# Kernel optimization log

Measured on AMD Instinct MI355X. Metric: run time of the kernel, lower is better.

## Reference

```python
import jax, jax.numpy as jnp
import numpy as np

C = 256
N_HEAD = 4
GROUPS = 32
EPS = 1e-5
B, H, W = 2, 64, 64


def group_norm(x, gamma, beta):
    # x: [B, C, H, W]; GroupNorm over (C//G, H, W) within each group
    b, c, h, w = x.shape
    xr = x.reshape(b, GROUPS, c // GROUPS, h, w)
    m = xr.mean(axis=(2, 3, 4), keepdims=True)
    v = xr.var(axis=(2, 3, 4), keepdims=True)
    xn = ((xr - m) * jax.lax.rsqrt(v + EPS)).reshape(b, c, h, w)
    return xn * gamma[None, :, None, None] + beta[None, :, None, None]


def setup_inputs() -> dict:
    key = jax.random.key(0)
    ks = jax.random.split(key, 5)
    s = 1.0 / np.sqrt(C)  # fan-in init scale for 1x1 convs
    return {
        "input": jax.random.normal(ks[0], (B, C, H, W), jnp.float32),
        "c": jax.random.normal(ks[1], (B, C, H, W), jnp.float32),
        "gn_w": jnp.ones((C,), jnp.float32),
        "gn_b": jnp.zeros((C,), jnp.float32),
        "wq": jax.random.normal(ks[2], (C, C), jnp.float32) * s,
        "wkv": jax.random.normal(ks[3], (2 * C, C), jnp.float32) * s,
        "wout_w": jax.random.normal(ks[4], (C, C), jnp.float32) * s,
        "wout_b": jnp.zeros((C,), jnp.float32),
    }


def reference(input, c, gn_w, gn_b, wq, wkv, wout_w, wout_b):
    b, ch, h, w = input.shape
    hd = ch // N_HEAD
    n = h * w
    # shared GroupNorm applied to both query source and context
    nq = group_norm(input, gn_w, gn_b)
    nkv = group_norm(c, gn_w, gn_b)
    # 1x1 convs == channel matmuls
    q = jnp.einsum('oc,bchw->bohw', wq, nq).reshape(b, N_HEAD, hd, n)
    kv = jnp.einsum('oc,bchw->bohw', wkv, nkv).reshape(b, N_HEAD, 2 * hd, n)
    k, v = jnp.split(kv, 2, axis=2)  # each [b, nh, hd, n]
    # NOTE: scale is 1/sqrt(channel), as in the source (not 1/sqrt(head_dim))
    attn = jnp.einsum('bncq,bnck->bnqk', q, k) / jnp.sqrt(jnp.float32(ch))
    attn = jax.nn.softmax(attn, axis=-1)
    o = jnp.einsum('bnqk,bnck->bncq', attn, v).reshape(b, ch, h, w)
    o = jnp.einsum('oc,bchw->bohw', wout_w, o) + wout_b[None, :, None, None]
    return o + input
```

## Files before the change

### kernel.cpp

```cpp
#include <hip/hip_runtime.h>


typedef __attribute__((ext_vector_type(8))) short short8;
typedef __attribute__((ext_vector_type(4))) short s4;
typedef __attribute__((ext_vector_type(4))) float f32x4;
typedef __attribute__((ext_vector_type(2))) unsigned int uint2v;

__device__ __forceinline__ unsigned short f2bf(float x) {
    unsigned int u = __builtin_bit_cast(unsigned int, x);
    u += 0x7FFFu + ((u >> 16) & 1u);
    return (unsigned short)(u >> 16);
}

__device__ __forceinline__ unsigned int pk2(float a, float b) {
    unsigned int ua = __builtin_bit_cast(unsigned int, a) + 0x8000u;
    unsigned int ub = __builtin_bit_cast(unsigned int, b) + 0x8000u;
    return (ua >> 16) | (ub & 0xFFFF0000u);
}

__device__ __forceinline__ short8 ld8(const unsigned short* p) {
    return *reinterpret_cast<const short8*>(p);
}

#define MFMA(a, b, c) __builtin_amdgcn_mfma_f32_16x16x32_bf16((a), (b), (c), 0, 0, 0)
#define MFMA16(a, b, c) __builtin_amdgcn_mfma_f32_16x16x16bf16_1k((a), (b), (c), 0, 0, 0)

__global__ __launch_bounds__(256) void wcvt(const float* __restrict__ wq,
                                            const float* __restrict__ wkv,
                                            const float* __restrict__ wo,
                                            unsigned short* __restrict__ dst) {
    int i = blockIdx.x * 256 + threadIdx.x;
    float v;
    if (i < 65536)       v = wq[i];
    else if (i < 196608) v = wkv[i - 65536];
    else                 v = wo[i - 196608];
    dst[i] = f2bf(v);
}

__global__ __launch_bounds__(256) void gnorm(const float* __restrict__ x0,
                                             const float* __restrict__ x1,
                                             unsigned short* __restrict__ d0,
                                             unsigned short* __restrict__ d1,
                                             const float* __restrict__ gamma,
                                             const float* __restrict__ beta) {
    int bid = blockIdx.x;
    const float* x = (bid & 64) ? x1 : x0;
    unsigned short* dst = (bid & 64) ? d1 : d0;
    int b = (bid >> 5) & 1, g = bid & 31;
    const float* base = x + (size_t)(b * 256 + g * 8) * 4096;
    int tid = threadIdx.x, lane = tid & 63, w = tid >> 6;

    float s = 0.f, s2 = 0.f;
    const float4* b4 = (const float4*)base;
    for (int i = tid; i < 8192; i += 256) {
        float4 v = b4[i];
        s  += v.x + v.y + v.z + v.w;
        s2 += v.x * v.x + v.y * v.y + v.z * v.z + v.w * v.w;
    }
    #pragma unroll
    for (int off = 32; off; off >>= 1) {
        s  += __shfl_down(s, off);
        s2 += __shfl_down(s2, off);
    }
    __shared__ float red[8];
    __shared__ float stat[2];
    if (lane == 0) { red[w] = s; red[4 + w] = s2; }
    __syncthreads();
    if (tid == 0) {
        float S = red[0] + red[1] + red[2] + red[3];
        float S2 = red[4] + red[5] + red[6] + red[7];
        float mean = S * (1.f / 32768.f);
        float var = S2 * (1.f / 32768.f) - mean * mean;
        stat[0] = mean;
        stat[1] = rsqrtf(var + 1e-5f);
    }
    __syncthreads();
    float mean = stat[0], inv = stat[1];

    float a[8], c0[8];
    #pragma unroll
    for (int cl = 0; cl < 8; cl++) {
        float gm = gamma[g * 8 + cl], bt = beta[g * 8 + cl];
        a[cl]  = gm * inv;
        c0[cl] = bt - mean * gm * inv;
    }
    for (int n = tid; n < 4096; n += 256) {
        unsigned short o[8];
        #pragma unroll
        for (int cl = 0; cl < 8; cl++) {
            float v = base[cl * 4096 + n];
            o[cl] = f2bf(v * a[cl] + c0[cl]);
        }
        *(uint4*)&dst[((size_t)(b * 4096 + n)) * 256 + g * 8] = *(const uint4*)o;
    }
}

__global__ __launch_bounds__(256) void proj_all(const unsigned short* __restrict__ nqT,
                                                const unsigned short* __restrict__ nkvT,
                                                const unsigned short* __restrict__ Wq,
                                                const unsigned short* __restrict__ Wkv,
                                                unsigned short* __restrict__ QT,
                                                unsigned short* __restrict__ KF,
                                                unsigned short* __restrict__ VF) {
    int bb = blockIdx.z;
    int y = blockIdx.y;
    bool isQ = (y < 4);
    int n0 = blockIdx.x * 128;
    int o0 = (isQ ? y : (y - 4)) * 64;
    int w = threadIdx.x >> 6, lane = threadIdx.x & 63;
    int m16 = lane & 15, g = lane >> 4;
    const unsigned short* Xb = (isQ ? nqT : nkvT) + (size_t)bb * 4096 * 256;
    const unsigned short* W = isQ ? Wq : Wkv;
    f32x4 acc[2][4] = {};
    int rowA = n0 + w * 32 + m16;
    #pragma unroll
    for (int k0 = 0; k0 < 256; k0 += 32) {
        short8 a0 = ld8(Xb + (size_t)rowA * 256 + k0 + g * 8);
        short8 a1 = ld8(Xb + (size_t)(rowA + 16) * 256 + k0 + g * 8);
        #pragma unroll
        for (int ct = 0; ct < 4; ct++) {
            short8 bf = ld8(W + (size_t)(o0 + ct * 16 + m16) * 256 + k0 + g * 8);
            acc[0][ct] = MFMA(a0, bf, acc[0][ct]);
            acc[1][ct] = MFMA(a1, bf, acc[1][ct]);
        }
    }
    if (isQ) {
        unsigned short* Ob = QT + (size_t)bb * 4096 * 256;
        #pragma unroll
        for (int mt = 0; mt < 2; mt++)
            #pragma unroll
            for (int ct = 0; ct < 4; ct++)
                #pragma unroll
                for (int r = 0; r < 4; r++) {
                    int n = n0 + w * 32 + mt * 16 + g * 4 + r;
                    int o = o0 + ct * 16 + m16;
                    Ob[(size_t)n * 256 + o] = f2bf(acc[mt][ct][r] * 0.0625f);
                }
    } else {
        int h2 = o0 >> 7, isV = (o0 >> 6) & 1;
        int bh = bb * 4 + h2;
        unsigned short* base = (isV ? VF : KF) + (size_t)bh * 262144;
        #pragma unroll
        for (int mt = 0; mt < 2; mt++)
            #pragma unroll
            for (int ct = 0; ct < 4; ct++)
                #pragma unroll
                for (int r = 0; r < 4; r++) {
                    int n = n0 + w * 32 + mt * 16 + g * 4 + r;
                    int c = ct * 16 + m16;
                    unsigned short v = f2bf(acc[mt][ct][r]);
                    size_t off;
                    if (isV) {
                        int T32 = n >> 5, kk5 = n & 31;
                        int gg = (kk5 & 15) >> 2;
                        int j = (kk5 & 3) + ((kk5 >> 4) << 2);
                        off = (((size_t)(T32 * 4 + ct)) * 64 + ((c & 15) + 16 * gg)) * 8 + j;
                    } else {
                        int T16 = n >> 4;
                        int cb = c >> 5, gg = (c >> 3) & 3, e = c & 7;
                        off = (((size_t)(T16 * 2 + cb)) * 64 + ((n & 15) + 16 * gg)) * 8 + e;
                    }
                    base[off] = v;
                }
    }
}

__global__ __launch_bounds__(512, 2) void attn(const unsigned short* __restrict__ QT,
                                               const unsigned short* __restrict__ KF,
                                               const unsigned short* __restrict__ VF,
                                               unsigned short* __restrict__ OT) {
    __shared__ unsigned short sm[32768];
    int bh = blockIdx.x & 7;
    int qb = blockIdx.x >> 3;
    int bb = bh >> 2, h = bh & 3;
    int tid = threadIdx.x;
    int w = tid >> 6, lane = tid & 63;
    int wq = w & 3, hh = w >> 2;
    int m16 = lane & 15, g = lane >> 4;
    int tloc = tid & 255;

    const unsigned short* KFb = KF + (size_t)bh * 262144;
    const unsigned short* VFb = VF + (size_t)bh * 262144;
    const unsigned short* Qb = QT + (size_t)bb * 4096 * 256;

    int q0 = qb * 64 + wq * 16;
    short8 bq0 = ld8(Qb + (size_t)(q0 + m16) * 256 + h * 64 + g * 8);
    short8 bq1 = ld8(Qb + (size_t)(q0 + m16) * 256 + h * 64 + 32 + g * 8);

    f32x4 acc[4] = {};
    float l = 0.f;

    {
        const uint4* ks = (const uint4*)(KFb + (size_t)(hh * 128) * 1024) + tloc;
        const uint4* vs = (const uint4*)(VFb + (size_t)(hh * 64) * 2048) + tloc;
        uint4 k0 = ks[0], k1 = ks[256], v0 = vs[0], v1 = vs[256];
        uint4* kd = (uint4*)(sm + (hh * 2) * 4096) + tloc;
        uint4* vd = (uint4*)(sm + 16384 + (hh * 2) * 4096) + tloc;
        kd[0] = k0; kd[256] = k1; vd[0] = v0; vd[256] = v1;
    }
    __syncthreads();

    for (int it = 0; it < 32; ++it) {
        int p = it & 1;
        bool pf = (it + 1 < 32);
        uint4 kp0, kp1, vp0, vp1;
        if (pf) {
            const uint4* ks = (const uint4*)(KFb + (size_t)(hh * 128 + (it + 1) * 4) * 1024) + tloc;
            const uint4* vs = (const uint4*)(VFb + (size_t)(hh * 64 + (it + 1) * 2) * 2048) + tloc;
            kp0 = ks[0]; kp1 = ks[256]; vp0 = vs[0]; vp1 = vs[256];
        }

        const unsigned short* Kbuf = sm + (hh * 2 + p) * 4096;
        const unsigned short* Vbuf = sm + 16384 + (hh * 2 + p) * 4096;

        s4 pb[4];
        #pragma unroll
        for (int t16 = 0; t16 < 4; t16++) {
            short8 a0 = ld8(Kbuf + (t16 * 2 + 0) * 512 + lane * 8);
            short8 a1 = ld8(Kbuf + (t16 * 2 + 1) * 512 + lane * 8);
            f32x4 st = {};
            st = MFMA(a0, bq0, st);
            st = MFMA(a1, bq1, st);
            #pragma unroll
            for (int r = 0; r < 4; r++) st[r] = __expf(st[r]);
            l += (st[0] + st[1]) + (st[2] + st[3]);
            uint2v wv; wv.x = pk2(st[0], st[1]); wv.y = pk2(st[2], st[3]);
            pb[t16] = __builtin_bit_cast(s4, wv);
        }
        #pragma unroll
        for (int T32 = 0; T32 < 2; T32++)
            #pragma unroll
            for (int dt = 0; dt < 4; dt++) {
                short8 va = ld8(Vbuf + (T32 * 4 + dt) * 512 + lane * 8);
                s4 va0 = __builtin_shufflevector(va, va, 0, 1, 2, 3);
                s4 va1 = __builtin_shufflevector(va, va, 4, 5, 6, 7);
                acc[dt] = MFMA16(va0, pb[T32 * 2], acc[dt]);
                acc[dt] = MFMA16(va1, pb[T32 * 2 + 1], acc[dt]);
            }

        if (pf) {
            uint4* kd = (uint4*)(sm + (hh * 2 + (p ^ 1)) * 4096) + tloc;
            uint4* vd = (uint4*)(sm + 16384 + (hh * 2 + (p ^ 1)) * 4096) + tloc;
            kd[0] = kp0; kd[256] = kp1; vd[0] = vp0; vd[256] = vp1;
        }
        __syncthreads();
    }

    l += __shfl_xor(l, 16);
    l += __shfl_xor(l, 32);

    float* Cf = (float*)sm;
    float* Lf = (float*)sm + 4096;
    if (hh == 1) {
        #pragma unroll
        for (int dt = 0; dt < 4; dt++)
            #pragma unroll
            for (int r = 0; r < 4; r++)
                Cf[wq * 1024 + (dt * 16 + g * 4 + r) * 16 + m16] = acc[dt][r];
        if (lane < 16) Lf[wq * 16 + m16] = l;
    }
    __syncthreads();
    if (hh == 0) {
        #pragma unroll
        for (int dt = 0; dt < 4; dt++)
            #pragma unroll
            for (int r = 0; r < 4; r++)
                acc[dt][r] += Cf[wq * 1024 + (dt * 16 + g * 4 + r) * 16 + m16];
        float invl = 1.f / (l + Lf[wq * 16 + m16]);
        unsigned short* Ob = OT + (size_t)bb * 4096 * 256;
        size_t obase = (size_t)(q0 + m16) * 256 + h * 64 + g * 4;
        #pragma unroll
        for (int dt = 0; dt < 4; dt++) {
            unsigned short o4[4];
            #pragma unroll
            for (int r = 0; r < 4; r++) o4[r] = f2bf(acc[dt][r] * invl);
            *(uint2*)&Ob[obase + dt * 16] = *(const uint2*)o4;
        }
    }
}

__global__ __launch_bounds__(256) void outproj(const unsigned short* __restrict__ Ot,
                                               const unsigned short* __restrict__ Wo,
                                               const float* __restrict__ bias,
                                               const float* __restrict__ resid,
                                               float* __restrict__ out) {
    int bb = blockIdx.z;
    int n0 = blockIdx.x * 128;
    int o0 = blockIdx.y * 64;
    int w = threadIdx.x >> 6, lane = threadIdx.x & 63;
    int m16 = lane & 15, g = lane >> 4;
    const unsigned short* Ob = Ot + (size_t)bb * 4096 * 256;
    int orow = o0 + w * 16 + m16;
    f32x4 acc[8] = {};
    #pragma unroll
    for (int k0 = 0; k0 < 256; k0 += 32) {
        short8 a = ld8(Wo + (size_t)orow * 256 + k0 + g * 8);
        #pragma unroll
        for (int ct = 0; ct < 8; ct++) {
            short8 bf = ld8(Ob + (size_t)(n0 + ct * 16 + m16) * 256 + k0 + g * 8);
            acc[ct] = MFMA(a, bf, acc[ct]);
        }
    }
    float biasr[4];
    #pragma unroll
    for (int r = 0; r < 4; r++) biasr[r] = bias[o0 + w * 16 + g * 4 + r];
    #pragma unroll
    for (int ct = 0; ct < 8; ct++)
        #pragma unroll
        for (int r = 0; r < 4; r++) {
            int o = o0 + w * 16 + g * 4 + r;
            int n = n0 + ct * 16 + m16;
            size_t idx = ((size_t)bb * 256 + o) * 4096 + n;
            out[idx] = acc[ct][r] + biasr[r] + resid[idx];
        }
}

extern "C" void kernel_launch(void* const* d_in, const int* in_sizes, int n_in,
                              void* d_out, int out_size, void* d_ws, size_t ws_size,
                              hipStream_t stream) {
    const float* input  = (const float*)d_in[0];
    const float* cctx   = (const float*)d_in[1];
    const float* gn_w   = (const float*)d_in[2];
    const float* gn_b   = (const float*)d_in[3];
    const float* wq     = (const float*)d_in[4];
    const float* wkv    = (const float*)d_in[5];
    const float* wout_w = (const float*)d_in[6];
    const float* wout_b = (const float*)d_in[7];
    float* out = (float*)d_out;

    unsigned short* ws = (unsigned short*)d_ws;
    unsigned short* wq_bf   = ws;
    unsigned short* wkv_bf  = ws + 65536;
    unsigned short* wout_bf = ws + 196608;
    unsigned short* nqT  = ws + 262144;
    unsigned short* nkvT = nqT + 2097152;
    unsigned short* QT   = nkvT + 2097152;
    unsigned short* KF   = QT + 2097152;
    unsigned short* VF   = KF + 2097152;
    unsigned short* OtT  = VF + 2097152;

    wcvt<<<1024, 256, 0, stream>>>(wq, wkv, wout_w, ws);
    gnorm<<<128, 256, 0, stream>>>(input, cctx, nqT, nkvT, gn_w, gn_b);
    proj_all<<<dim3(32, 12, 2), 256, 0, stream>>>(nqT, nkvT, wq_bf, wkv_bf, QT, KF, VF);
    attn<<<512, 512, 0, stream>>>(QT, KF, VF, OtT);
    outproj<<<dim3(32, 4, 2), 256, 0, stream>>>(OtT, wout_bf, wout_b, input, out);
}
```

Measured before the change: 200.2 us.

## Split groupnorm into atomic stats pass, fuse weight conversion, restructure attention waves

GroupNorm becomes two kernels: a 4x wider stats pass that accumulates sums with atomics, and a normalize pass, to raise parallelism over the former 128-block kernel. The standalone weight conversion kernel is removed, and each projection block converts its fp32 weight tile into padded LDS instead. Attention drops to 256 threads per block with each wave handling two query tiles, reusing K/V fragments, and switches to exp2f with log2e folded into the Q scale. The output projection tile shrinks to 64 columns to launch more blocks. These changes add a memset launch and redundant per-block weight conversion work.

```diff
diff --git a/kernel.cpp b/kernel.cpp
--- a/kernel.cpp
+++ b/kernel.cpp
@@ -25,35 +25,18 @@
 #define MFMA(a, b, c) __builtin_amdgcn_mfma_f32_16x16x32_bf16((a), (b), (c), 0, 0, 0)
 #define MFMA16(a, b, c) __builtin_amdgcn_mfma_f32_16x16x16bf16_1k((a), (b), (c), 0, 0, 0)
 
-__global__ __launch_bounds__(256) void wcvt(const float* __restrict__ wq,
-                                            const float* __restrict__ wkv,
-                                            const float* __restrict__ wo,
-                                            unsigned short* __restrict__ dst) {
-    int i = blockIdx.x * 256 + threadIdx.x;
-    float v;
-    if (i < 65536)       v = wq[i];
-    else if (i < 196608) v = wkv[i - 65536];
-    else                 v = wo[i - 196608];
-    dst[i] = f2bf(v);
-}
-
-__global__ __launch_bounds__(256) void gnorm(const float* __restrict__ x0,
-                                             const float* __restrict__ x1,
-                                             unsigned short* __restrict__ d0,
-                                             unsigned short* __restrict__ d1,
-                                             const float* __restrict__ gamma,
-                                             const float* __restrict__ beta) {
-    int bid = blockIdx.x;
-    const float* x = (bid & 64) ? x1 : x0;
-    unsigned short* dst = (bid & 64) ? d1 : d0;
-    int b = (bid >> 5) & 1, g = bid & 31;
-    const float* base = x + (size_t)(b * 256 + g * 8) * 4096;
+__global__ __launch_bounds__(256) void gn_stats(const float* __restrict__ x0,
+                                                const float* __restrict__ x1,
+                                                float* __restrict__ statw) {
+    int blk = blockIdx.x;
+    int combo = blk >> 2, chunk = blk & 3;
+    const float* x = (combo & 64) ? x1 : x0;
+    int b = (combo >> 5) & 1, g = combo & 31;
+    const float4* base = (const float4*)(x + (size_t)(b * 256 + g * 8) * 4096) + chunk * 2048;
     int tid = threadIdx.x, lane = tid & 63, w = tid >> 6;
-
     float s = 0.f, s2 = 0.f;
-    const float4* b4 = (const float4*)base;
-    for (int i = tid; i < 8192; i += 256) {
-        float4 v = b4[i];
+    for (int i = tid; i < 2048; i += 256) {
+        float4 v = base[i];
         s  += v.x + v.y + v.z + v.w;
         s2 += v.x * v.x + v.y * v.y + v.z * v.z + v.w * v.w;
     }
@@ -63,20 +46,30 @@
         s2 += __shfl_down(s2, off);
     }
     __shared__ float red[8];
-    __shared__ float stat[2];
     if (lane == 0) { red[w] = s; red[4 + w] = s2; }
     __syncthreads();
     if (tid == 0) {
-        float S = red[0] + red[1] + red[2] + red[3];
-        float S2 = red[4] + red[5] + red[6] + red[7];
-        float mean = S * (1.f / 32768.f);
-        float var = S2 * (1.f / 32768.f) - mean * mean;
-        stat[0] = mean;
-        stat[1] = rsqrtf(var + 1e-5f);
-    }
-    __syncthreads();
-    float mean = stat[0], inv = stat[1];
-
+        atomicAdd(&statw[combo * 2],     red[0] + red[1] + red[2] + red[3]);
+        atomicAdd(&statw[combo * 2 + 1], red[4] + red[5] + red[6] + red[7]);
+    }
+}
+
+__global__ __launch_bounds__(256) void gn_norm(const float* __restrict__ x0,
+                                               const float* __restrict__ x1,
+                                               unsigned short* __restrict__ d0,
+                                               unsigned short* __restrict__ d1,
+                                               const float* __restrict__ statw,
+                                               const float* __restrict__ gamma,
+                                               const float* __restrict__ beta) {
+    int blk = blockIdx.x;
+    int combo = blk >> 2, chunk = blk & 3;
+    const float* x = (combo & 64) ? x1 : x0;
+    unsigned short* dst = (combo & 64) ? d1 : d0;
+    int b = (combo >> 5) & 1, g = combo & 31;
+    const float* base = x + (size_t)(b * 256 + g * 8) * 4096;
+    float mean = statw[combo * 2] * (1.f / 32768.f);
+    float var = statw[combo * 2 + 1] * (1.f / 32768.f) - mean * mean;
+    float inv = rsqrtf(var + 1e-5f);
     float a[8], c0[8];
     #pragma unroll
     for (int cl = 0; cl < 8; cl++) {
@@ -84,7 +77,7 @@
         a[cl]  = gm * inv;
         c0[cl] = bt - mean * gm * inv;
     }
-    for (int n = tid; n < 4096; n += 256) {
+    for (int n = chunk * 1024 + threadIdx.x; n < (chunk + 1) * 1024; n += 256) {
         unsigned short o[8];
         #pragma unroll
         for (int cl = 0; cl < 8; cl++) {
@@ -97,20 +90,35 @@
 
 __global__ __launch_bounds__(256) void proj_all(const unsigned short* __restrict__ nqT,
                                                 const unsigned short* __restrict__ nkvT,
-                                                const unsigned short* __restrict__ Wq,
-                                                const unsigned short* __restrict__ Wkv,
+                                                const float* __restrict__ Wq,
+                                                const float* __restrict__ Wkv,
                                                 unsigned short* __restrict__ QT,
                                                 unsigned short* __restrict__ KF,
                                                 unsigned short* __restrict__ VF) {
+    __shared__ unsigned short Wl[64 * 264];
     int bb = blockIdx.z;
     int y = blockIdx.y;
     bool isQ = (y < 4);
     int n0 = blockIdx.x * 128;
     int o0 = (isQ ? y : (y - 4)) * 64;
-    int w = threadIdx.x >> 6, lane = threadIdx.x & 63;
+    int tid = threadIdx.x;
+    int w = tid >> 6, lane = tid & 63;
     int m16 = lane & 15, g = lane >> 4;
+
+    {
+        const float* Wsrc = (isQ ? Wq : Wkv) + (size_t)o0 * 256;
+        int row = tid >> 2, c4 = (tid & 3) * 16;
+        const float4* wr = (const float4*)(Wsrc + (size_t)row * 256) + c4;
+        #pragma unroll
+        for (int j = 0; j < 16; j++) {
+            float4 v = wr[j];
+            unsigned short o4[4] = {f2bf(v.x), f2bf(v.y), f2bf(v.z), f2bf(v.w)};
+            *(uint2*)&Wl[row * 264 + (c4 + j) * 4] = *(const uint2*)o4;
+        }
+    }
+    __syncthreads();
+
     const unsigned short* Xb = (isQ ? nqT : nkvT) + (size_t)bb * 4096 * 256;
-    const unsigned short* W = isQ ? Wq : Wkv;
     f32x4 acc[2][4] = {};
     int rowA = n0 + w * 32 + m16;
     #pragma unroll
@@ -119,12 +127,13 @@
         short8 a1 = ld8(Xb + (size_t)(rowA + 16) * 256 + k0 + g * 8);
         #pragma unroll
         for (int ct = 0; ct < 4; ct++) {
-            short8 bf = ld8(W + (size_t)(o0 + ct * 16 + m16) * 256 + k0 + g * 8);
+            short8 bf = ld8(&Wl[(ct * 16 + m16) * 264 + k0 + g * 8]);
             acc[0][ct] = MFMA(a0, bf, acc[0][ct]);
             acc[1][ct] = MFMA(a1, bf, acc[1][ct]);
         }
     }
     if (isQ) {
+        const float qs = 0.09016844005556021f;
         unsigned short* Ob = QT + (size_t)bb * 4096 * 256;
         #pragma unroll
         for (int mt = 0; mt < 2; mt++)
@@ -134,7 +143,7 @@
                 for (int r = 0; r < 4; r++) {
                     int n = n0 + w * 32 + mt * 16 + g * 4 + r;
                     int o = o0 + ct * 16 + m16;
-                    Ob[(size_t)n * 256 + o] = f2bf(acc[mt][ct][r] * 0.0625f);
+                    Ob[(size_t)n * 256 + o] = f2bf(acc[mt][ct][r] * qs);
                 }
     } else {
         int h2 = o0 >> 7, isV = (o0 >> 6) & 1;
@@ -165,7 +174,7 @@
     }
 }
 
-__global__ __launch_bounds__(512, 2) void attn(const unsigned short* __restrict__ QT,
+__global__ __launch_bounds__(256, 2) void attn(const unsigned short* __restrict__ QT,
                                                const unsigned short* __restrict__ KF,
                                                const unsigned short* __restrict__ VF,
                                                unsigned short* __restrict__ OT) {
@@ -175,57 +184,68 @@
     int bb = bh >> 2, h = bh & 3;
     int tid = threadIdx.x;
     int w = tid >> 6, lane = tid & 63;
-    int wq = w & 3, hh = w >> 2;
+    int wq = w & 1, hh = w >> 1;
     int m16 = lane & 15, g = lane >> 4;
-    int tloc = tid & 255;
 
     const unsigned short* KFb = KF + (size_t)bh * 262144;
     const unsigned short* VFb = VF + (size_t)bh * 262144;
     const unsigned short* Qb = QT + (size_t)bb * 4096 * 256;
 
-    int q0 = qb * 64 + wq * 16;
-    short8 bq0 = ld8(Qb + (size_t)(q0 + m16) * 256 + h * 64 + g * 8);
-    short8 bq1 = ld8(Qb + (size_t)(q0 + m16) * 256 + h * 64 + 32 + g * 8);
-
-    f32x4 acc[4] = {};
-    float l = 0.f;
+    int q0 = qb * 64 + wq * 32;
+    short8 bq0A = ld8(Qb + (size_t)(q0 + m16) * 256 + h * 64 + g * 8);
+    short8 bq1A = ld8(Qb + (size_t)(q0 + m16) * 256 + h * 64 + 32 + g * 8);
+    short8 bq0B = ld8(Qb + (size_t)(q0 + 16 + m16) * 256 + h * 64 + g * 8);
+    short8 bq1B = ld8(Qb + (size_t)(q0 + 16 + m16) * 256 + h * 64 + 32 + g * 8);
+
+    f32x4 accA[4] = {}, accB[4] = {};
+    f32x4 l4A = {}, l4B = {};
+
+    int sh = tid >> 7;
+    int st = tid & 127;
 
     {
-        const uint4* ks = (const uint4*)(KFb + (size_t)(hh * 128) * 1024) + tloc;
-        const uint4* vs = (const uint4*)(VFb + (size_t)(hh * 64) * 2048) + tloc;
-        uint4 k0 = ks[0], k1 = ks[256], v0 = vs[0], v1 = vs[256];
-        uint4* kd = (uint4*)(sm + (hh * 2) * 4096) + tloc;
-        uint4* vd = (uint4*)(sm + 16384 + (hh * 2) * 4096) + tloc;
-        kd[0] = k0; kd[256] = k1; vd[0] = v0; vd[256] = v1;
+        const uint4* ks = (const uint4*)KFb + (size_t)(sh * 128) * 128 + st;
+        const uint4* vs = (const uint4*)VFb + (size_t)(sh * 64) * 256 + st;
+        uint4* kd = (uint4*)(sm + (sh * 2) * 4096) + st;
+        uint4* vd = (uint4*)(sm + 16384 + (sh * 2) * 4096) + st;
+        #pragma unroll
+        for (int j = 0; j < 4; j++) kd[j * 128] = ks[j * 128];
+        #pragma unroll
+        for (int j = 0; j < 4; j++) vd[j * 128] = vs[j * 128];
     }
     __syncthreads();
 
     for (int it = 0; it < 32; ++it) {
         int p = it & 1;
         bool pf = (it + 1 < 32);
-        uint4 kp0, kp1, vp0, vp1;
+        uint4 kp[4], vp[4];
         if (pf) {
-            const uint4* ks = (const uint4*)(KFb + (size_t)(hh * 128 + (it + 1) * 4) * 1024) + tloc;
-            const uint4* vs = (const uint4*)(VFb + (size_t)(hh * 64 + (it + 1) * 2) * 2048) + tloc;
-            kp0 = ks[0]; kp1 = ks[256]; vp0 = vs[0]; vp1 = vs[256];
+            const uint4* ks = (const uint4*)KFb + (size_t)(sh * 128 + (it + 1) * 4) * 128 + st;
+            const uint4* vs = (const uint4*)VFb + (size_t)(sh * 64 + (it + 1) * 2) * 256 + st;
+            #pragma unroll
+            for (int j = 0; j < 4; j++) kp[j] = ks[j * 128];
+            #pragma unroll
+            for (int j = 0; j < 4; j++) vp[j] = vs[j * 128];
         }
 
         const unsigned short* Kbuf = sm + (hh * 2 + p) * 4096;
         const unsigned short* Vbuf = sm + 16384 + (hh * 2 + p) * 4096;
 
-        s4 pb[4];
+        s4 pbA[4], pbB[4];
         #pragma unroll
         for (int t16 = 0; t16 < 4; t16++) {
             short8 a0 = ld8(Kbuf + (t16 * 2 + 0) * 512 + lane * 8);
             short8 a1 = ld8(Kbuf + (t16 * 2 + 1) * 512 + lane * 8);
-            f32x4 st = {};
-            st = MFMA(a0, bq0, st);
-            st = MFMA(a1, bq1, st);
-            #pragma unroll
-            for (int r = 0; r < 4; r++) st[r] = __expf(st[r]);
-            l += (st[0] + st[1]) + (st[2] + st[3]);
-            uint2v wv; wv.x = pk2(st[0], st[1]); wv.y = pk2(st[2], st[3]);
-            pb[t16] = __builtin_bit_cast(s4, wv);
+            f32x4 sA = {}, sB = {};
+            sA = MFMA(a0, bq0A, sA); sA = MFMA(a1, bq1A, sA);
+            sB = MFMA(a0, bq0B, sB); sB = MFMA(a1, bq1B, sB);
+            #pragma unroll
+            for (int r = 0; r < 4; r++) { sA[r] = exp2f(sA[r]); sB[r] = exp2f(sB[r]); }
+            l4A += sA; l4B += sB;
+            uint2v wA; wA.x = pk2(sA[0], sA[1]); wA.y = pk2(sA[2], sA[3]);
+            uint2v wB; wB.x = pk2(sB[0], sB[1]); wB.y = pk2(sB[2], sB[3]);
+            pbA[t16] = __builtin_bit_cast(s4, wA);
+            pbB[t16] = __builtin_bit_cast(s4, wB);
         }
         #pragma unroll
         for (int T32 = 0; T32 < 2; T32++)
@@ -234,20 +254,27 @@
                 short8 va = ld8(Vbuf + (T32 * 4 + dt) * 512 + lane * 8);
                 s4 va0 = __builtin_shufflevector(va, va, 0, 1, 2, 3);
                 s4 va1 = __builtin_shufflevector(va, va, 4, 5, 6, 7);
-                acc[dt] = MFMA16(va0, pb[T32 * 2], acc[dt]);
-                acc[dt] = MFMA16(va1, pb[T32 * 2 + 1], acc[dt]);
+                accA[dt] = MFMA16(va0, pbA[T32 * 2], accA[dt]);
+                accA[dt] = MFMA16(va1, pbA[T32 * 2 + 1], accA[dt]);
+                accB[dt] = MFMA16(va0, pbB[T32 * 2], accB[dt]);
+                accB[dt] = MFMA16(va1, pbB[T32 * 2 + 1], accB[dt]);
             }
 
         if (pf) {
-            uint4* kd = (uint4*)(sm + (hh * 2 + (p ^ 1)) * 4096) + tloc;
-            uint4* vd = (uint4*)(sm + 16384 + (hh * 2 + (p ^ 1)) * 4096) + tloc;
-            kd[0] = kp0; kd[256] = kp1; vd[0] = vp0; vd[256] = vp1;
+            uint4* kd = (uint4*)(sm + (sh * 2 + (p ^ 1)) * 4096) + st;
+            uint4* vd = (uint4*)(sm + 16384 + (sh * 2 + (p ^ 1)) * 4096) + st;
+            #pragma unroll
+            for (int j = 0; j < 4; j++) kd[j * 128] = kp[j];
+            #pragma unroll
+            for (int j = 0; j < 4; j++) vd[j * 128] = vp[j];
         }
         __syncthreads();
     }
 
-    l += __shfl_xor(l, 16);
-    l += __shfl_xor(l, 32);
+    float lA = (l4A[0] + l4A[1]) + (l4A[2] + l4A[3]);
+    float lB = (l4B[0] + l4B[1]) + (l4B[2] + l4B[3]);
+    lA += __shfl_xor(lA, 16); lA += __shfl_xor(lA, 32);
+    lB += __shfl_xor(lB, 16); lB += __shfl_xor(lB, 32);
 
     float* Cf = (float*)sm;
     float* Lf = (float*)sm + 4096;
@@ -255,48 +282,77 @@
         #pragma unroll
         for (int dt = 0; dt < 4; dt++)
             #pragma unroll
-            for (int r = 0; r < 4; r++)
-                Cf[wq * 1024 + (dt * 16 + g * 4 + r) * 16 + m16] = acc[dt][r];
-        if (lane < 16) Lf[wq * 16 + m16] = l;
+            for (int r = 0; r < 4; r++) {
+                int d = dt * 16 + g * 4 + r;
+                Cf[((wq * 2 + 0) * 64 + d) * 16 + m16] = accA[dt][r];
+                Cf[((wq * 2 + 1) * 64 + d) * 16 + m16] = accB[dt][r];
+            }
+        if (lane < 16) {
+            Lf[(wq * 2 + 0) * 16 + m16] = lA;
+            Lf[(wq * 2 + 1) * 16 + m16] = lB;
+        }
     }
     __syncthreads();
     if (hh == 0) {
         #pragma unroll
         for (int dt = 0; dt < 4; dt++)
             #pragma unroll
-            for (int r = 0; r < 4; r++)
-                acc[dt][r] += Cf[wq * 1024 + (dt * 16 + g * 4 + r) * 16 + m16];
-        float invl = 1.f / (l + Lf[wq * 16 + m16]);
+            for (int r = 0; r < 4; r++) {
+                int d = dt * 16 + g * 4 + r;
+                accA[dt][r] += Cf[((wq * 2 + 0) * 64 + d) * 16 + m16];
+                accB[dt][r] += Cf[((wq * 2 + 1) * 64 + d) * 16 + m16];
+            }
+        float invlA = 1.f / (lA + Lf[(wq * 2 + 0) * 16 + m16]);
+        float invlB = 1.f / (lB + Lf[(wq * 2 + 1) * 16 + m16]);
         unsigned short* Ob = OT + (size_t)bb * 4096 * 256;
-        size_t obase = (size_t)(q0 + m16) * 256 + h * 64 + g * 4;
+        size_t obA = (size_t)(q0 + m16) * 256 + h * 64 + g * 4;
+        size_t obB = (size_t)(q0 + 16 + m16) * 256 + h * 64 + g * 4;
         #pragma unroll
         for (int dt = 0; dt < 4; dt++) {
             unsigned short o4[4];
             #pragma unroll
-            for (int r = 0; r < 4; r++) o4[r] = f2bf(acc[dt][r] * invl);
-            *(uint2*)&Ob[obase + dt * 16] = *(const uint2*)o4;
+            for (int r = 0; r < 4; r++) o4[r] = f2bf(accA[dt][r] * invlA);
+            *(uint2*)&Ob[obA + dt * 16] = *(const uint2*)o4;
+            #pragma unroll
+            for (int r = 0; r < 4; r++) o4[r] = f2bf(accB[dt][r] * invlB);
+            *(uint2*)&Ob[obB + dt * 16] = *(const uint2*)o4;
         }
     }
 }
 
 __global__ __launch_bounds__(256) void outproj(const unsigned short* __restrict__ Ot,
-                                               const unsigned short* __restrict__ Wo,
+                                               const float* __restrict__ Wo,
                                                const float* __restrict__ bias,
                                                const float* __restrict__ resid,
                                                float* __restrict__ out) {
+    __shared__ unsigned short Wl[64 * 264];
     int bb = blockIdx.z;
-    int n0 = blockIdx.x * 128;
+    int n0 = blockIdx.x * 64;
     int o0 = blockIdx.y * 64;
-    int w = threadIdx.x >> 6, lane = threadIdx.x & 63;
+    int tid = threadIdx.x;
+    int w = tid >> 6, lane = tid & 63;
     int m16 = lane & 15, g = lane >> 4;
+
+    {
+        const float* Wsrc = Wo + (size_t)o0 * 256;
+        int row = tid >> 2, c4 = (tid & 3) * 16;
+        const float4* wr = (const float4*)(Wsrc + (size_t)row * 256) + c4;
+        #pragma unroll
+        for (int j = 0; j < 16; j++) {
+            float4 v = wr[j];
+            unsigned short o4[4] = {f2bf(v.x), f2bf(v.y), f2bf(v.z), f2bf(v.w)};
+            *(uint2*)&Wl[row * 264 + (c4 + j) * 4] = *(const uint2*)o4;
+        }
+    }
+    __syncthreads();
+
     const unsigned short* Ob = Ot + (size_t)bb * 4096 * 256;
-    int orow = o0 + w * 16 + m16;
-    f32x4 acc[8] = {};
+    f32x4 acc[4] = {};
     #pragma unroll
     for (int k0 = 0; k0 < 256; k0 += 32) {
-        short8 a = ld8(Wo + (size_t)orow * 256 + k0 + g * 8);
-        #pragma unroll
-        for (int ct = 0; ct < 8; ct++) {
+        short8 a = ld8(&Wl[(w * 16 + m16) * 264 + k0 + g * 8]);
+        #pragma unroll
+        for (int ct = 0; ct < 4; ct++) {
             short8 bf = ld8(Ob + (size_t)(n0 + ct * 16 + m16) * 256 + k0 + g * 8);
             acc[ct] = MFMA(a, bf, acc[ct]);
         }
@@ -305,7 +361,7 @@
     #pragma unroll
     for (int r = 0; r < 4; r++) biasr[r] = bias[o0 + w * 16 + g * 4 + r];
     #pragma unroll
-    for (int ct = 0; ct < 8; ct++)
+    for (int ct = 0; ct < 4; ct++)
         #pragma unroll
         for (int r = 0; r < 4; r++) {
             int o = o0 + w * 16 + g * 4 + r;
@@ -329,19 +385,18 @@
     float* out = (float*)d_out;
 
     unsigned short* ws = (unsigned short*)d_ws;
-    unsigned short* wq_bf   = ws;
-    unsigned short* wkv_bf  = ws + 65536;
-    unsigned short* wout_bf = ws + 196608;
-    unsigned short* nqT  = ws + 262144;
+    unsigned short* nqT  = ws;
     unsigned short* nkvT = nqT + 2097152;
     unsigned short* QT   = nkvT + 2097152;
     unsigned short* KF   = QT + 2097152;
     unsigned short* VF   = KF + 2097152;
     unsigned short* OtT  = VF + 2097152;
-
-    wcvt<<<1024, 256, 0, stream>>>(wq, wkv, wout_w, ws);
-    gnorm<<<128, 256, 0, stream>>>(input, cctx, nqT, nkvT, gn_w, gn_b);
-    proj_all<<<dim3(32, 12, 2), 256, 0, stream>>>(nqT, nkvT, wq_bf, wkv_bf, QT, KF, VF);
-    attn<<<512, 512, 0, stream>>>(QT, KF, VF, OtT);
-    outproj<<<dim3(32, 4, 2), 256, 0, stream>>>(OtT, wout_bf, wout_b, input, out);
-}
+    float* statw = (float*)(OtT + 2097152);
+
+    hipMemsetAsync(statw, 0, 256 * sizeof(float), stream);
+    gn_stats<<<512, 256, 0, stream>>>(input, cctx, statw);
+    gn_norm<<<512, 256, 0, stream>>>(input, cctx, nqT, nkvT, statw, gn_w, gn_b);
+    proj_all<<<dim3(32, 12, 2), 256, 0, stream>>>(nqT, nkvT, wq, wkv, QT, KF, VF);
+    attn<<<512, 256, 0, stream>>>(QT, KF, VF, OtT);
+    outproj<<<dim3(64, 4, 2), 256, 0, stream>>>(OtT, wout_w, wout_b, input, out);
+}
```

Measured after the change: 204.0 us. About the same (+1.9%).

## Split GroupNorm into parallel stats and LDS-transposed normalize, fuse weight conversion

Applied to the files above, without the earlier changes.

Splits GroupNorm into a 512-block partial-statistics pass and a 256-block normalize pass that transposes through swizzled LDS for coalesced writes. This replaces the old 128-block kernel that issued strided stores. The separate weight-conversion kernel is removed; proj_all and outproj now convert their fp32 weight tiles to bf16 in LDS. The softmax switches to exp2 by folding log2(e) into the Q scale, and outproj uses smaller tiles to launch more blocks. Costs are redundant per-block weight conversion and an extra launch for the statistics pass.

```diff
diff --git a/kernel.cpp b/kernel.cpp
--- a/kernel.cpp
+++ b/kernel.cpp
@@ -25,35 +25,18 @@
 #define MFMA(a, b, c) __builtin_amdgcn_mfma_f32_16x16x32_bf16((a), (b), (c), 0, 0, 0)
 #define MFMA16(a, b, c) __builtin_amdgcn_mfma_f32_16x16x16bf16_1k((a), (b), (c), 0, 0, 0)
 
-__global__ __launch_bounds__(256) void wcvt(const float* __restrict__ wq,
-                                            const float* __restrict__ wkv,
-                                            const float* __restrict__ wo,
-                                            unsigned short* __restrict__ dst) {
-    int i = blockIdx.x * 256 + threadIdx.x;
-    float v;
-    if (i < 65536)       v = wq[i];
-    else if (i < 196608) v = wkv[i - 65536];
-    else                 v = wo[i - 196608];
-    dst[i] = f2bf(v);
-}
-
-__global__ __launch_bounds__(256) void gnorm(const float* __restrict__ x0,
-                                             const float* __restrict__ x1,
-                                             unsigned short* __restrict__ d0,
-                                             unsigned short* __restrict__ d1,
-                                             const float* __restrict__ gamma,
-                                             const float* __restrict__ beta) {
-    int bid = blockIdx.x;
-    const float* x = (bid & 64) ? x1 : x0;
-    unsigned short* dst = (bid & 64) ? d1 : d0;
-    int b = (bid >> 5) & 1, g = bid & 31;
-    const float* base = x + (size_t)(b * 256 + g * 8) * 4096;
+__global__ __launch_bounds__(256) void gn_stats(const float* __restrict__ x0,
+                                                const float* __restrict__ x1,
+                                                float* __restrict__ statw) {
+    int blk = blockIdx.x;
+    int combo = blk >> 2, chunk = blk & 3;
+    const float* x = (combo & 64) ? x1 : x0;
+    int b = (combo >> 5) & 1, g = combo & 31;
+    const float4* base = (const float4*)(x + (size_t)(b * 256 + g * 8) * 4096) + chunk * 2048;
     int tid = threadIdx.x, lane = tid & 63, w = tid >> 6;
-
     float s = 0.f, s2 = 0.f;
-    const float4* b4 = (const float4*)base;
-    for (int i = tid; i < 8192; i += 256) {
-        float4 v = b4[i];
+    for (int i = tid; i < 2048; i += 256) {
+        float4 v = base[i];
         s  += v.x + v.y + v.z + v.w;
         s2 += v.x * v.x + v.y * v.y + v.z * v.z + v.w * v.w;
     }
@@ -63,54 +46,98 @@
         s2 += __shfl_down(s2, off);
     }
     __shared__ float red[8];
-    __shared__ float stat[2];
     if (lane == 0) { red[w] = s; red[4 + w] = s2; }
     __syncthreads();
     if (tid == 0) {
-        float S = red[0] + red[1] + red[2] + red[3];
-        float S2 = red[4] + red[5] + red[6] + red[7];
+        float* o = statw + (size_t)(combo * 4 + chunk) * 2;
+        o[0] = red[0] + red[1] + red[2] + red[3];
+        o[1] = red[4] + red[5] + red[6] + red[7];
+    }
+}
+
+__global__ __launch_bounds__(256) void gn_norm(const float* __restrict__ x0,
+                                               const float* __restrict__ x1,
+                                               unsigned short* __restrict__ d0,
+                                               unsigned short* __restrict__ d1,
+                                               const float* __restrict__ statw,
+                                               const float* __restrict__ gamma,
+                                               const float* __restrict__ beta) {
+    __shared__ unsigned short Xl[64 * 272];
+    __shared__ float aL[256], bL[256];
+    int blk = blockIdx.x;
+    int t = blk >> 7, b = (blk >> 6) & 1, n0 = (blk & 63) * 64;
+    const float* x = t ? x1 : x0;
+    unsigned short* dst = t ? d1 : d0;
+    int tid = threadIdx.x;
+    {
+        int c = tid, g = c >> 3;
+        int combo = (t << 6) | (b << 5) | g;
+        const float* sw = statw + (size_t)combo * 8;
+        float S  = (sw[0] + sw[2]) + (sw[4] + sw[6]);
+        float S2 = (sw[1] + sw[3]) + (sw[5] + sw[7]);
         float mean = S * (1.f / 32768.f);
         float var = S2 * (1.f / 32768.f) - mean * mean;
-        stat[0] = mean;
-        stat[1] = rsqrtf(var + 1e-5f);
-    }
-    __syncthreads();
-    float mean = stat[0], inv = stat[1];
-
-    float a[8], c0[8];
-    #pragma unroll
-    for (int cl = 0; cl < 8; cl++) {
-        float gm = gamma[g * 8 + cl], bt = beta[g * 8 + cl];
-        a[cl]  = gm * inv;
-        c0[cl] = bt - mean * gm * inv;
-    }
-    for (int n = tid; n < 4096; n += 256) {
-        unsigned short o[8];
-        #pragma unroll
-        for (int cl = 0; cl < 8; cl++) {
-            float v = base[cl * 4096 + n];
-            o[cl] = f2bf(v * a[cl] + c0[cl]);
-        }
-        *(uint4*)&dst[((size_t)(b * 4096 + n)) * 256 + g * 8] = *(const uint4*)o;
+        float inv = rsqrtf(var + 1e-5f);
+        float gm = gamma[c];
+        aL[c] = gm * inv;
+        bL[c] = beta[c] - mean * gm * inv;
+    }
+    __syncthreads();
+    const float* xb = x + (size_t)b * 256 * 4096 + n0;
+    #pragma unroll
+    for (int it = 0; it < 16; it++) {
+        int c = it * 16 + (tid >> 4);
+        int n4 = tid & 15;
+        float4 v = *(const float4*)(xb + (size_t)c * 4096 + n4 * 4);
+        float a = aL[c], c0 = bL[c];
+        int cs = c ^ ((n4 & 7) << 3);
+        Xl[(n4 * 4 + 0) * 272 + cs] = f2bf(v.x * a + c0);
+        Xl[(n4 * 4 + 1) * 272 + cs] = f2bf(v.y * a + c0);
+        Xl[(n4 * 4 + 2) * 272 + cs] = f2bf(v.z * a + c0);
+        Xl[(n4 * 4 + 3) * 272 + cs] = f2bf(v.w * a + c0);
+    }
+    __syncthreads();
+    int n = tid >> 2, co = (tid & 3) * 64;
+    int key = ((n >> 2) & 7) << 3;
+    unsigned short* drow = dst + (size_t)(b * 4096 + n0 + n) * 256 + co;
+    #pragma unroll
+    for (int j = 0; j < 8; j++) {
+        int src = n * 272 + ((co + j * 8) ^ key);
+        *(uint4*)(drow + j * 8) = *(const uint4*)&Xl[src];
     }
 }
 
 __global__ __launch_bounds__(256) void proj_all(const unsigned short* __restrict__ nqT,
                                                 const unsigned short* __restrict__ nkvT,
-                                                const unsigned short* __restrict__ Wq,
-                                                const unsigned short* __restrict__ Wkv,
+                                                const float* __restrict__ Wq,
+                                                const float* __restrict__ Wkv,
                                                 unsigned short* __restrict__ QT,
                                                 unsigned short* __restrict__ KF,
                                                 unsigned short* __restrict__ VF) {
+    __shared__ unsigned short Wl[64 * 264];
     int bb = blockIdx.z;
     int y = blockIdx.y;
     bool isQ = (y < 4);
     int n0 = blockIdx.x * 128;
     int o0 = (isQ ? y : (y - 4)) * 64;
-    int w = threadIdx.x >> 6, lane = threadIdx.x & 63;
+    int tid = threadIdx.x;
+    int w = tid >> 6, lane = tid & 63;
     int m16 = lane & 15, g = lane >> 4;
+
+    {
+        const float* Wsrc = (isQ ? Wq : Wkv) + (size_t)o0 * 256;
+        int row = tid >> 2, c4 = (tid & 3) * 16;
+        const float4* wr = (const float4*)(Wsrc + (size_t)row * 256) + c4;
+        #pragma unroll
+        for (int j = 0; j < 16; j++) {
+            float4 v = wr[j];
+            unsigned short o4[4] = {f2bf(v.x), f2bf(v.y), f2bf(v.z), f2bf(v.w)};
+            *(uint2*)&Wl[row * 264 + (c4 + j) * 4] = *(const uint2*)o4;
+        }
+    }
+    __syncthreads();
+
     const unsigned short* Xb = (isQ ? nqT : nkvT) + (size_t)bb * 4096 * 256;
-    const unsigned short* W = isQ ? Wq : Wkv;
     f32x4 acc[2][4] = {};
     int rowA = n0 + w * 32 + m16;
     #pragma unroll
@@ -119,12 +146,13 @@
         short8 a1 = ld8(Xb + (size_t)(rowA + 16) * 256 + k0 + g * 8);
         #pragma unroll
         for (int ct = 0; ct < 4; ct++) {
-            short8 bf = ld8(W + (size_t)(o0 + ct * 16 + m16) * 256 + k0 + g * 8);
+            short8 bf = ld8(&Wl[(ct * 16 + m16) * 264 + k0 + g * 8]);
             acc[0][ct] = MFMA(a0, bf, acc[0][ct]);
             acc[1][ct] = MFMA(a1, bf, acc[1][ct]);
         }
     }
     if (isQ) {
+        const float qs = 0.09016844005556021f;
         unsigned short* Ob = QT + (size_t)bb * 4096 * 256;
         #pragma unroll
         for (int mt = 0; mt < 2; mt++)
@@ -134,7 +162,7 @@
                 for (int r = 0; r < 4; r++) {
                     int n = n0 + w * 32 + mt * 16 + g * 4 + r;
                     int o = o0 + ct * 16 + m16;
-                    Ob[(size_t)n * 256 + o] = f2bf(acc[mt][ct][r] * 0.0625f);
+                    Ob[(size_t)n * 256 + o] = f2bf(acc[mt][ct][r] * qs);
                 }
     } else {
         int h2 = o0 >> 7, isV = (o0 >> 6) & 1;
@@ -222,7 +250,7 @@
             st = MFMA(a0, bq0, st);
             st = MFMA(a1, bq1, st);
             #pragma unroll
-            for (int r = 0; r < 4; r++) st[r] = __expf(st[r]);
+            for (int r = 0; r < 4; r++) st[r] = exp2f(st[r]);
             l += (st[0] + st[1]) + (st[2] + st[3]);
             uint2v wv; wv.x = pk2(st[0], st[1]); wv.y = pk2(st[2], st[3]);
             pb[t16] = __builtin_bit_cast(s4, wv);
@@ -280,23 +308,38 @@
 }
 
 __global__ __launch_bounds__(256) void outproj(const unsigned short* __restrict__ Ot,
-                                               const unsigned short* __restrict__ Wo,
+                                               const float* __restrict__ Wo,
                                                const float* __restrict__ bias,
                                                const float* __restrict__ resid,
                                                float* __restrict__ out) {
+    __shared__ unsigned short Wl[64 * 264];
     int bb = blockIdx.z;
-    int n0 = blockIdx.x * 128;
+    int n0 = blockIdx.x * 64;
     int o0 = blockIdx.y * 64;
-    int w = threadIdx.x >> 6, lane = threadIdx.x & 63;
+    int tid = threadIdx.x;
+    int w = tid >> 6, lane = tid & 63;
     int m16 = lane & 15, g = lane >> 4;
+
+    {
+        const float* Wsrc = Wo + (size_t)o0 * 256;
+        int row = tid >> 2, c4 = (tid & 3) * 16;
+        const float4* wr = (const float4*)(Wsrc + (size_t)row * 256) + c4;
+        #pragma unroll
+        for (int j = 0; j < 16; j++) {
+            float4 v = wr[j];
+            unsigned short o4[4] = {f2bf(v.x), f2bf(v.y), f2bf(v.z), f2bf(v.w)};
+            *(uint2*)&Wl[row * 264 + (c4 + j) * 4] = *(const uint2*)o4;
+        }
+    }
+    __syncthreads();
+
     const unsigned short* Ob = Ot + (size_t)bb * 4096 * 256;
-    int orow = o0 + w * 16 + m16;
-    f32x4 acc[8] = {};
+    f32x4 acc[4] = {};
     #pragma unroll
     for (int k0 = 0; k0 < 256; k0 += 32) {
-        short8 a = ld8(Wo + (size_t)orow * 256 + k0 + g * 8);
-        #pragma unroll
-        for (int ct = 0; ct < 8; ct++) {
+        short8 a = ld8(&Wl[(w * 16 + m16) * 264 + k0 + g * 8]);
+        #pragma unroll
+        for (int ct = 0; ct < 4; ct++) {
             short8 bf = ld8(Ob + (size_t)(n0 + ct * 16 + m16) * 256 + k0 + g * 8);
             acc[ct] = MFMA(a, bf, acc[ct]);
         }
@@ -305,7 +348,7 @@
     #pragma unroll
     for (int r = 0; r < 4; r++) biasr[r] = bias[o0 + w * 16 + g * 4 + r];
     #pragma unroll
-    for (int ct = 0; ct < 8; ct++)
+    for (int ct = 0; ct < 4; ct++)
         #pragma unroll
         for (int r = 0; r < 4; r++) {
             int o = o0 + w * 16 + g * 4 + r;
@@ -329,19 +372,17 @@
     float* out = (float*)d_out;
 
     unsigned short* ws = (unsigned short*)d_ws;
-    unsigned short* wq_bf   = ws;
-    unsigned short* wkv_bf  = ws + 65536;
-    unsigned short* wout_bf = ws + 196608;
-    unsigned short* nqT  = ws + 262144;
+    unsigned short* nqT  = ws;
     unsigned short* nkvT = nqT + 2097152;
     unsigned short* QT   = nkvT + 2097152;
     unsigned short* KF   = QT + 2097152;
     unsigned short* VF   = KF + 2097152;
     unsigned short* OtT  = VF + 2097152;
-
-    wcvt<<<1024, 256, 0, stream>>>(wq, wkv, wout_w, ws);
-    gnorm<<<128, 256, 0, stream>>>(input, cctx, nqT, nkvT, gn_w, gn_b);
-    proj_all<<<dim3(32, 12, 2), 256, 0, stream>>>(nqT, nkvT, wq_bf, wkv_bf, QT, KF, VF);
+    float* statw = (float*)(OtT + 2097152);
+
+    gn_stats<<<512, 256, 0, stream>>>(input, cctx, statw);
+    gn_norm<<<256, 256, 0, stream>>>(input, cctx, nqT, nkvT, statw, gn_w, gn_b);
+    proj_all<<<dim3(32, 12, 2), 256, 0, stream>>>(nqT, nkvT, wq, wkv, QT, KF, VF);
     attn<<<512, 512, 0, stream>>>(QT, KF, VF, OtT);
-    outproj<<<dim3(32, 4, 2), 256, 0, stream>>>(OtT, wout_bf, wout_b, input, out);
-}
+    outproj<<<dim3(64, 4, 2), 256, 0, stream>>>(OtT, wout_w, wout_b, input, out);
+}
```

Result: faster. 182.0 us (-9.1%).
